# Performance work log

Hardware: AMD Instinct MI355X
Metric: run time of the kernel (lower is better)

The kernel has to match this reference:

```python
import jax, jax.numpy as jnp
import numpy as np

B, S, HID = 1, 2048, 2048
H, KVH, D, VD = 32, 8, 128, 128
R = 64  # rope_dim = head_dim * partial_rotary_factor, rounded down to even
N_REP = H // KVH
SCALE = D ** -0.5
NEG = -1e9


def _rotate_half(x):
    half = x.shape[-1] // 2
    return jnp.concatenate([-x[..., half:], x[..., :half]], axis=-1)


def setup_inputs() -> dict:
    key = jax.random.key(0)
    ks = jax.random.split(key, 8)
    hidden_states = jax.random.normal(ks[0], (B, S, HID), dtype=jnp.float32)
    # RoPE angles: standard inverse-frequency positional embedding of width R
    inv_freq = 1.0 / (10000.0 ** (np.arange(0, R, 2, dtype=np.float32) / R))
    pos = np.arange(S, dtype=np.float32)
    freqs = np.outer(pos, inv_freq)                       # [S, R/2]
    emb = np.concatenate([freqs, freqs], axis=-1)         # [S, R]
    cos = jnp.asarray(np.cos(emb))[None].repeat(B, axis=0)  # [B, S, R]
    sin = jnp.asarray(np.sin(emb))[None].repeat(B, axis=0)
    # additive causal mask [B, 1, S, S]
    causal = jnp.triu(jnp.full((S, S), NEG, dtype=jnp.float32), k=1)
    attention_mask = jnp.broadcast_to(causal[None, None], (B, 1, S, S))
    std = 0.02
    Wq = jax.random.normal(ks[1], (H * D, HID), dtype=jnp.float32) * std
    Wk = jax.random.normal(ks[2], (KVH * D, HID), dtype=jnp.float32) * std
    Wv = jax.random.normal(ks[3], (KVH * VD, HID), dtype=jnp.float32) * std
    Wo = jax.random.normal(ks[4], (HID, H * VD), dtype=jnp.float32) * std
    sink_bias = jax.random.normal(ks[5], (H,), dtype=jnp.float32) * 0.5
    return {"hidden_states": hidden_states, "cos": cos, "sin": sin,
            "attention_mask": attention_mask, "Wq": Wq, "Wk": Wk, "Wv": Wv,
            "Wo": Wo, "sink_bias": sink_bias}


def reference(hidden_states, cos, sin, attention_mask, Wq, Wk, Wv, Wo, sink_bias):
    b, s, _ = hidden_states.shape
    # projections -> [B, heads, S, dim]
    q = (hidden_states @ Wq.T).reshape(b, s, H, D).transpose(0, 2, 1, 3)
    k = (hidden_states @ Wk.T).reshape(b, s, KVH, D).transpose(0, 2, 1, 3)
    v = (hidden_states @ Wv.T).reshape(b, s, KVH, VD).transpose(0, 2, 1, 3)
    # partial RoPE on first R dims
    c = cos[:, None, :, :]  # [B,1,S,R]
    si = sin[:, None, :, :]
    q_r, q_n = q[..., :R], q[..., R:]
    k_r, k_n = k[..., :R], k[..., R:]
    q = jnp.concatenate([q_r * c + _rotate_half(q_r) * si, q_n], axis=-1)
    k = jnp.concatenate([k_r * c + _rotate_half(k_r) * si, k_n], axis=-1)
    # GQA: repeat kv heads
    k_rep = jnp.repeat(k, N_REP, axis=1)
    v_rep = jnp.repeat(v, N_REP, axis=1)
    scores = jnp.einsum('bhqd,bhkd->bhqk', q, k_rep) * SCALE + attention_mask
    # extra attention-sink logit column per head
    sinks = jnp.broadcast_to(sink_bias.reshape(1, H, 1, 1), (b, H, s, 1))
    aw = jnp.concatenate([scores, sinks], axis=-1)            # [B,H,S,S+1]
    probs = jax.nn.softmax(aw, axis=-1)[..., :-1]             # drop sink column
    out = jnp.einsum('bhqk,bhkd->bhqd', probs, v_rep)
    out = out.transpose(0, 2, 1, 3).reshape(b, s, H * VD)
    return out @ Wo.T
```

## Files before the change

### kernel.cpp

```cpp
#include <hip/hip_runtime.h>

typedef unsigned short u16;
typedef unsigned int   u32;
typedef __bf16  bf16x8 __attribute__((ext_vector_type(8)));
typedef float   f32x4  __attribute__((ext_vector_type(4)));
typedef float   f32x16 __attribute__((ext_vector_type(16)));
typedef u16     u16x4  __attribute__((ext_vector_type(4)));
typedef u16     u16x8  __attribute__((ext_vector_type(8)));
typedef u32     u32x4  __attribute__((ext_vector_type(4)));

#define S_LEN 2048
#define NH 32
#define NKVH 8
#define HD 128
#define QKVST 6144
#define AOST  4096
#define ATT_SCALE 0.08838834764831845f
#define LOG2E 1.4426950408889634f
#define QSC2 (ATT_SCALE * LOG2E)
#define RESCALE_THR2 11.5f

__device__ __forceinline__ u16 f2bf(float f){
  u32 u = __builtin_bit_cast(u32, f);
  u += 0x7FFFu + ((u >> 16) & 1u);
  return (u16)(u >> 16);
}
__device__ __forceinline__ u32 cvtpk(float lo, float hi){
  u32 d;
  asm("v_cvt_pk_bf16_f32 %0, %1, %2" : "=v"(d) : "v"(lo), "v"(hi));
  return d;
}
__device__ __forceinline__ void gload_lds16(const u16* g, u16* l){
  __builtin_amdgcn_global_load_lds(
      (const __attribute__((address_space(1))) void*)g,
      (__attribute__((address_space(3))) void*)l, 16, 0, 0);
}

__global__ void cvt_all_kernel(const f32x4* __restrict__ hs, const f32x4* __restrict__ wq,
                               const f32x4* __restrict__ wk, const f32x4* __restrict__ wv,
                               const f32x4* __restrict__ wo, u16x4* __restrict__ out){
  int i = blockIdx.x * 256 + threadIdx.x;
  const f32x4* src; int off;
  if      (i < 1048576){ src = hs; off = i; }
  else if (i < 3145728){ src = wq; off = i - 1048576; }
  else if (i < 3670016){ src = wk; off = i - 3145728; }
  else if (i < 4194304){ src = wv; off = i - 3670016; }
  else                 { src = wo; off = i - 4194304; }
  f32x4 v = src[off];
  u16x4 o;
  o[0] = f2bf(v[0]); o[1] = f2bf(v[1]); o[2] = f2bf(v[2]); o[3] = f2bf(v[3]);
  out[i] = o;
}

template<int OUT_BF16, int ROPE, int BM, int BN, int BK>
__global__ __launch_bounds__(256, 2)
void gemm_bt_kernel(const u16* __restrict__ X, const u16* __restrict__ W,
                    void* __restrict__ Cv, int M, int N, int K,
                    const float* __restrict__ cosv, const float* __restrict__ sinv){
  const int NS = BK / 32;
  __shared__ __align__(16) u16 As[2][NS][BM * 32];
  __shared__ __align__(16) u16 Bs[2][NS][BN * 32];
  const int MI = BM / 32, NJ = BN / 32;
  const int m0 = blockIdx.y * BM, n0 = blockIdx.x * BN;
  const int tid = threadIdx.x;
  const int wave = tid >> 6, lane = tid & 63;
  const int wm = wave >> 1, wn = wave & 1;
  const int g = lane >> 4, ln = lane & 15;
  const int r0 = tid >> 2;
  const int cc = (tid & 3) * 8;
  f32x4 acc[MI][NJ] = {};
  const u16* xa0 = X + (size_t)(m0 + r0) * K + cc;
  const u16* xa1 = X + (size_t)(m0 + r0 + 64) * K + cc;
  const u16* wb0 = W + (size_t)(n0 + r0) * K + cc;
  const u16* wb1 = W + (size_t)(n0 + r0 + 64) * K + cc;

  auto stage = [&](int buf, int k0){
    #pragma unroll
    for (int s = 0; s < NS; s++){
      const int kc = k0 + s * 32;
      gload_lds16(xa0 + kc, &As[buf][s][tid * 8]);
      if (BM == 128) gload_lds16(xa1 + kc, &As[buf][s][2048 + tid * 8]);
      gload_lds16(wb0 + kc, &Bs[buf][s][tid * 8]);
      if (BN == 128) gload_lds16(wb1 + kc, &Bs[buf][s][2048 + tid * 8]);
    }
  };

  stage(0, 0);
  __syncthreads();
  int cur = 0;
  for (int k0 = 0; k0 < K; k0 += BK){
    if (k0 + BK < K) stage(cur ^ 1, k0 + BK);
    #pragma unroll
    for (int s = 0; s < NS; s++){
      bf16x8 a[MI], b[NJ];
      #pragma unroll
      for (int f = 0; f < MI; f++) a[f] = *(const bf16x8*)&As[cur][s][(wm * (BM / 2) + f * 16 + ln) * 32 + g * 8];
      #pragma unroll
      for (int f = 0; f < NJ; f++) b[f] = *(const bf16x8*)&Bs[cur][s][(wn * (BN / 2) + f * 16 + ln) * 32 + g * 8];
      __builtin_amdgcn_s_setprio(1);
      #pragma unroll
      for (int i = 0; i < MI; i++)
        #pragma unroll
        for (int j = 0; j < NJ; j++)
          acc[i][j] = __builtin_amdgcn_mfma_f32_16x16x32_bf16(a[i], b[j], acc[i][j], 0, 0, 0);
      __builtin_amdgcn_s_setprio(0);
    }
    __syncthreads();
    cur ^= 1;
  }
  if (ROPE && BN == 128){
    if (wn == 0 && n0 < 5120){
      #pragma unroll
      for (int i = 0; i < MI; i++)
        #pragma unroll
        for (int r = 0; r < 4; r++){
          const int row = m0 + wm * (BM / 2) + i * 16 + g * 4 + r;
          #pragma unroll
          for (int j = 0; j < 2; j++){
            const int d = j * 16 + ln;
            float c  = cosv[row * 64 + d];
            float sn = sinv[row * 64 + d];
            float x0 = acc[i][j][r], x1 = acc[i][j + 2][r];
            acc[i][j][r]     = x0 * c - x1 * sn;
            acc[i][j + 2][r] = x1 * c + x0 * sn;
          }
        }
    }
    if (n0 < 4096){
      #pragma unroll
      for (int i = 0; i < MI; i++)
        #pragma unroll
        for (int j = 0; j < NJ; j++)
          #pragma unroll
          for (int r = 0; r < 4; r++) acc[i][j][r] *= QSC2;
    }
  }
  #pragma unroll
  for (int i = 0; i < MI; i++)
    #pragma unroll
    for (int j = 0; j < NJ; j++)
      #pragma unroll
      for (int r = 0; r < 4; r++){
        int row = m0 + wm * (BM / 2) + i * 16 + g * 4 + r;
        int col = n0 + wn * (BN / 2) + j * 16 + ln;
        if (OUT_BF16) ((u16*)Cv)[(size_t)row * N + col] = f2bf(acc[i][j][r]);
        else          ((float*)Cv)[(size_t)row * N + col] = acc[i][j][r];
      }
}

__global__ void vtrans_kernel(const u16* __restrict__ QKV, u16* __restrict__ VT){
  int idx = blockIdx.x * 256 + threadIdx.x;
  if (idx >= NKVH * HD * S_LEN) return;
  int s   = idx & (S_LEN - 1);
  int vd  = (idx >> 11) & (HD - 1);
  int kvh = idx >> 18;
  VT[idx] = QKV[(size_t)s * QKVST + 5120 + kvh * HD + vd];
}

__global__ __launch_bounds__(256, 2)
void attn_kernel(const u16* __restrict__ QKV, const u16* __restrict__ VT,
                 const float* __restrict__ sinkb, u16* __restrict__ AO){
  __shared__ __align__(16) u16 Ks[2][32 * 256];
  __shared__ __align__(16) u16 Vs[2][32 * 256];
  const int b    = blockIdx.x;
  const int kvh  = b & 7;
  const int head = kvh * 4 + ((b >> 3) & 3);
  const int slot = b >> 5;
  const int qt   = (slot < 8) ? (15 - slot) : (slot - 8);
  const int tid  = threadIdx.x;
  const int w    = tid >> 6;
  const int lane = tid & 63;
  const int l31  = lane & 31, hi = lane >> 5;
  const int q0   = qt * 128;
  const int qw   = q0 + w * 32;

  const u16* Kbase = QKV + 4096 + kvh * HD;
  const u16* Vbase = VT + (size_t)kvh * HD * S_LEN;

  auto stage = [&](int buf, int kt){
    const int k0 = kt * 64;
    #pragma unroll
    for (int p = 0; p < 4; p++){
      int idx = p * 256 + tid;
      int r = idx >> 5, c = idx & 31;
      int cs = c ^ r;
      int key = r * 2 + (cs >> 4), d8 = (cs & 15) * 8;
      gload_lds16(Kbase + (size_t)(k0 + key) * QKVST + d8, &Ks[buf][idx * 8]);
    }
    #pragma unroll
    for (int p = 0; p < 4; p++){
      int idx = p * 256 + tid;
      int r = idx >> 5, c = idx & 31;
      int cs = c ^ r;
      int vd = r * 4 + (cs >> 3), k8 = (cs & 7) * 8;
      gload_lds16(Vbase + (size_t)vd * S_LEN + k0 + k8, &Vs[buf][idx * 8]);
    }
  };

  bf16x8 qB[8];
  const u16* qrow = QKV + (size_t)(qw + l31) * QKVST + head * HD;
  #pragma unroll
  for (int t = 0; t < 8; t++) qB[t] = *(const bf16x8*)(qrow + t * 16 + hi * 8);

  float m  = sinkb[head] * LOG2E;
  float Ll = (hi == 0) ? 1.f : 0.f;
  f32x16 O[4] = {};

  const int nkt = 2 * qt + 2;
  stage(0, 0);
  __syncthreads();
  int cur = 0;

  for (int kt = 0; kt < nkt; kt++){
    const int k0 = kt * 64;
    if (kt + 1 < nkt) stage(cur ^ 1, kt + 1);

    if (k0 < qw + 32){
      const u16* Kc = Ks[cur];
      const u16* Vc = Vs[cur];
      f32x16 sc0 = {}, sc1 = {};
      const int krow0 = (l31 >> 1);
      const int kc0   = ((l31 & 1) << 4) | hi;
      __builtin_amdgcn_s_setprio(1);
      #pragma unroll
      for (int t = 0; t < 8; t++){
        bf16x8 ka0 = *(const bf16x8*)&Kc[krow0 * 256 + ((kc0 + 2 * t) ^ krow0) * 8];
        bf16x8 ka1 = *(const bf16x8*)&Kc[(16 + krow0) * 256 + ((kc0 + 2 * t) ^ (16 + krow0)) * 8];
        sc0 = __builtin_amdgcn_mfma_f32_32x32x16_bf16(ka0, qB[t], sc0, 0, 0, 0);
        sc1 = __builtin_amdgcn_mfma_f32_32x32x16_bf16(ka1, qB[t], sc1, 0, 0, 0);
      }
      __builtin_amdgcn_s_setprio(0);

      if (k0 + 63 > qw){
        const int qg = qw + l31;
        #pragma unroll
        for (int r = 0; r < 16; r++){
          int keyr = k0 + (r & 3) + 8 * (r >> 2) + 4 * hi;
          if (keyr      > qg) sc0[r] = -1e30f;
          if (keyr + 32 > qg) sc1[r] = -1e30f;
        }
      }
      float mx = sc0[0];
      #pragma unroll
      for (int r = 1; r < 16; r++) mx = fmaxf(mx, sc0[r]);
      #pragma unroll
      for (int r = 0; r < 16; r++) mx = fmaxf(mx, sc1[r]);
      mx = fmaxf(mx, __shfl_xor(mx, 32));
      if (!__all(mx <= m + RESCALE_THR2)){
        float mn = fmaxf(m, mx);
        float sf = exp2f(m - mn);
        m = mn;
        #pragma unroll
        for (int n = 0; n < 4; n++)
          #pragma unroll
          for (int r = 0; r < 16; r++) O[n][r] *= sf;
        Ll *= sf;
      }
      float p0[16], p1[16];
      #pragma unroll
      for (int r = 0; r < 16; r++){ p0[r] = exp2f(sc0[r] - m); Ll += p0[r]; }
      #pragma unroll
      for (int r = 0; r < 16; r++){ p1[r] = exp2f(sc1[r] - m); Ll += p1[r]; }

      __builtin_amdgcn_s_setprio(1);
      #pragma unroll
      for (int c = 0; c < 4; c++){
        const float* ps = (c & 2) ? p1 : p0;
        const int bb = (c & 1) * 8;
        u32 wa = cvtpk(ps[bb + 0], ps[bb + 1]);
        u32 wb = cvtpk(ps[bb + 2], ps[bb + 3]);
        u32 wc = cvtpk(ps[bb + 4], ps[bb + 5]);
        u32 wd = cvtpk(ps[bb + 6], ps[bb + 7]);
        asm("v_permlane32_swap_b32 %0, %1" : "+v"(wa), "+v"(wc));
        asm("v_permlane32_swap_b32 %0, %1" : "+v"(wb), "+v"(wd));
        u32x4 wv_; wv_[0] = wa; wv_[1] = wb; wv_[2] = wc; wv_[3] = wd;
        bf16x8 pf = __builtin_bit_cast(bf16x8, wv_);
        #pragma unroll
        for (int n = 0; n < 4; n++){
          const int vrow = n * 8 + (l31 >> 2);
          const int vcc  = ((l31 & 3) << 3) | (c << 1) | hi;
          bf16x8 va = *(const bf16x8*)&Vc[vrow * 256 + (vcc ^ vrow) * 8];
          O[n] = __builtin_amdgcn_mfma_f32_32x32x16_bf16(va, pf, O[n], 0, 0, 0);
        }
      }
      __builtin_amdgcn_s_setprio(0);
    }
    __syncthreads();
    cur ^= 1;
  }

  float l = Ll + __shfl_xor(Ll, 32);
  float inv = 1.f / l;
  u16* arena = &Ks[0][0];
  #pragma unroll
  for (int n = 0; n < 4; n++)
    #pragma unroll
    for (int r = 0; r < 16; r++){
      int vd = n * 32 + (r & 3) + 8 * (r >> 2) + 4 * hi;
      int ch = (vd >> 3) ^ (l31 & 15);
      arena[w * 4096 + l31 * 128 + ch * 8 + (vd & 7)] = f2bf(O[n][r] * inv);
    }
  __syncthreads();
  #pragma unroll
  for (int p = 0; p < 8; p++){
    int idx = p * 256 + tid;
    int row = idx >> 4, c = idx & 15;
    u16x8 v = *(const u16x8*)&arena[row * 128 + ((c ^ (row & 15)) * 8)];
    *(u16x8*)&AO[(size_t)(q0 + row) * AOST + head * HD + c * 8] = v;
  }
}

extern "C" void kernel_launch(void* const* d_in, const int* in_sizes, int n_in,
                              void* d_out, int out_size, void* d_ws, size_t ws_size,
                              hipStream_t stream){
  (void)in_sizes; (void)n_in; (void)out_size; (void)ws_size;
  const float* hs    = (const float*)d_in[0];
  const float* cosv  = (const float*)d_in[1];
  const float* sinv  = (const float*)d_in[2];
  const float* Wq    = (const float*)d_in[4];
  const float* Wk    = (const float*)d_in[5];
  const float* Wv    = (const float*)d_in[6];
  const float* Wo    = (const float*)d_in[7];
  const float* sinkb = (const float*)d_in[8];
  float* out = (float*)d_out;

  char* ws = (char*)d_ws;
  u16* XB    = (u16*)(ws);
  u16* WQKVB = (u16*)(ws + 8388608);
  u16* WOB   = (u16*)(ws + 33554432);
  u16* QKV   = (u16*)(ws + 50331648);
  u16* VT    = (u16*)(ws + 75497472);
  u16* AO    = (u16*)(ws + 79691776);

  cvt_all_kernel<<<24576, 256, 0, stream>>>((const f32x4*)hs, (const f32x4*)Wq,
                                            (const f32x4*)Wk, (const f32x4*)Wv,
                                            (const f32x4*)Wo, (u16x4*)ws);

  gemm_bt_kernel<1, 1, 128, 128, 32><<<dim3(48, 16), 256, 0, stream>>>(XB, WQKVB, QKV, 2048, 6144, 2048, cosv, sinv);

  vtrans_kernel<<<8192, 256, 0, stream>>>(QKV, VT);

  attn_kernel<<<dim3(512), 256, 0, stream>>>(QKV, VT, sinkb, AO);

  gemm_bt_kernel<0, 0, 128, 64, 64><<<dim3(32, 16), 256, 0, stream>>>(AO, WOB, out, 2048, 2048, 4096, nullptr, nullptr);
}
```

Before: 229.3 us.

## Split long causal query tiles across blocks with LSE merge for load balance

Each attention block now does a fixed amount of work. The long query tiles (qt 8..15) are split along the key dimension: one block handles keys 0..17 tiles and a second block handles the rest, then the second block also processes a short tile. The partial outputs are written in bf16 together with per-row log-sum-exp values into workspace reused from the XB area. A new merge kernel combines the two partials. This is meant to remove the tail imbalance of the causal workload, at the cost of an extra kernel launch, partial-output traffic and additional bf16 rounding.

```diff
diff --git a/kernel.cpp b/kernel.cpp
--- a/kernel.cpp
+++ b/kernel.cpp
@@ -19,11 +19,16 @@
 #define LOG2E 1.4426950408889634f
 #define QSC2 (ATT_SCALE * LOG2E)
 #define RESCALE_THR2 11.5f
+#define PARTSZ 16640
 
 __device__ __forceinline__ u16 f2bf(float f){
   u32 u = __builtin_bit_cast(u32, f);
   u += 0x7FFFu + ((u >> 16) & 1u);
   return (u16)(u >> 16);
+}
+__device__ __forceinline__ float bf2f(u16 h){
+  u32 u = ((u32)h) << 16;
+  return __builtin_bit_cast(float, u);
 }
 __device__ __forceinline__ u32 cvtpk(float lo, float hi){
   u32 d;
@@ -159,20 +164,20 @@
 
 __global__ __launch_bounds__(256, 2)
 void attn_kernel(const u16* __restrict__ QKV, const u16* __restrict__ VT,
-                 const float* __restrict__ sinkb, u16* __restrict__ AO){
+                 const float* __restrict__ sinkb, u16* __restrict__ AO,
+                 u16* __restrict__ PART){
   __shared__ __align__(16) u16 Ks[2][32 * 256];
   __shared__ __align__(16) u16 Vs[2][32 * 256];
   const int b    = blockIdx.x;
   const int kvh  = b & 7;
   const int head = kvh * 4 + ((b >> 3) & 3);
-  const int slot = b >> 5;
-  const int qt   = (slot < 8) ? (15 - slot) : (slot - 8);
+  const int p    = (b >> 5) & 7;
+  const int role = b >> 8;
+  const int qtL  = 15 - p;
   const int tid  = threadIdx.x;
   const int w    = tid >> 6;
   const int lane = tid & 63;
   const int l31  = lane & 31, hi = lane >> 5;
-  const int q0   = qt * 128;
-  const int qw   = q0 + w * 32;
 
   const u16* Kbase = QKV + 4096 + kvh * HD;
   const u16* Vbase = VT + (size_t)kvh * HD * S_LEN;
@@ -180,16 +185,16 @@
   auto stage = [&](int buf, int kt){
     const int k0 = kt * 64;
     #pragma unroll
-    for (int p = 0; p < 4; p++){
-      int idx = p * 256 + tid;
+    for (int pp = 0; pp < 4; pp++){
+      int idx = pp * 256 + tid;
       int r = idx >> 5, c = idx & 31;
       int cs = c ^ r;
       int key = r * 2 + (cs >> 4), d8 = (cs & 15) * 8;
       gload_lds16(Kbase + (size_t)(k0 + key) * QKVST + d8, &Ks[buf][idx * 8]);
     }
     #pragma unroll
-    for (int p = 0; p < 4; p++){
-      int idx = p * 256 + tid;
+    for (int pp = 0; pp < 4; pp++){
+      int idx = pp * 256 + tid;
       int r = idx >> 5, c = idx & 31;
       int cs = c ^ r;
       int vd = r * 4 + (cs >> 3), k8 = (cs & 7) * 8;
@@ -197,116 +202,183 @@
     }
   };
 
+  const float sb2 = sinkb[head] * LOG2E;
   bf16x8 qB[8];
-  const u16* qrow = QKV + (size_t)(qw + l31) * QKVST + head * HD;
+  float m, Ll;
+  f32x16 O[4];
+
+  auto load_q = [&](int q0){
+    const int qw = q0 + w * 32;
+    const u16* qrow = QKV + (size_t)(qw + l31) * QKVST + head * HD;
+    #pragma unroll
+    for (int t = 0; t < 8; t++) qB[t] = *(const bf16x8*)(qrow + t * 16 + hi * 8);
+    #pragma unroll
+    for (int n = 0; n < 4; n++) O[n] = f32x16{};
+  };
+
+  auto do_tile = [&](int cur, int k0, int qw){
+    const u16* Kc = Ks[cur];
+    const u16* Vc = Vs[cur];
+    f32x16 sc0 = {}, sc1 = {};
+    const int krow0 = (l31 >> 1);
+    const int kc0   = ((l31 & 1) << 4) | hi;
+    __builtin_amdgcn_s_setprio(1);
+    #pragma unroll
+    for (int t = 0; t < 8; t++){
+      bf16x8 ka0 = *(const bf16x8*)&Kc[krow0 * 256 + ((kc0 + 2 * t) ^ krow0) * 8];
+      bf16x8 ka1 = *(const bf16x8*)&Kc[(16 + krow0) * 256 + ((kc0 + 2 * t) ^ (16 + krow0)) * 8];
+      sc0 = __builtin_amdgcn_mfma_f32_32x32x16_bf16(ka0, qB[t], sc0, 0, 0, 0);
+      sc1 = __builtin_amdgcn_mfma_f32_32x32x16_bf16(ka1, qB[t], sc1, 0, 0, 0);
+    }
+    __builtin_amdgcn_s_setprio(0);
+
+    if (k0 + 63 > qw){
+      const int qg = qw + l31;
+      #pragma unroll
+      for (int r = 0; r < 16; r++){
+        int keyr = k0 + (r & 3) + 8 * (r >> 2) + 4 * hi;
+        if (keyr      > qg) sc0[r] = -1e30f;
+        if (keyr + 32 > qg) sc1[r] = -1e30f;
+      }
+    }
+    float mx = sc0[0];
+    #pragma unroll
+    for (int r = 1; r < 16; r++) mx = fmaxf(mx, sc0[r]);
+    #pragma unroll
+    for (int r = 0; r < 16; r++) mx = fmaxf(mx, sc1[r]);
+    mx = fmaxf(mx, __shfl_xor(mx, 32));
+    if (!__all(mx <= m + RESCALE_THR2)){
+      float mn = fmaxf(m, mx);
+      float sf = exp2f(m - mn);
+      m = mn;
+      #pragma unroll
+      for (int n = 0; n < 4; n++)
+        #pragma unroll
+        for (int r = 0; r < 16; r++) O[n][r] *= sf;
+      Ll *= sf;
+    }
+    float p0[16], p1[16];
+    #pragma unroll
+    for (int r = 0; r < 16; r++){ p0[r] = exp2f(sc0[r] - m); Ll += p0[r]; }
+    #pragma unroll
+    for (int r = 0; r < 16; r++){ p1[r] = exp2f(sc1[r] - m); Ll += p1[r]; }
+
+    __builtin_amdgcn_s_setprio(1);
+    #pragma unroll
+    for (int c = 0; c < 4; c++){
+      const float* ps = (c & 2) ? p1 : p0;
+      const int bb = (c & 1) * 8;
+      u32 wa = cvtpk(ps[bb + 0], ps[bb + 1]);
+      u32 wb = cvtpk(ps[bb + 2], ps[bb + 3]);
+      u32 wc = cvtpk(ps[bb + 4], ps[bb + 5]);
+      u32 wd = cvtpk(ps[bb + 6], ps[bb + 7]);
+      asm("v_permlane32_swap_b32 %0, %1" : "+v"(wa), "+v"(wc));
+      asm("v_permlane32_swap_b32 %0, %1" : "+v"(wb), "+v"(wd));
+      u32x4 wv_; wv_[0] = wa; wv_[1] = wb; wv_[2] = wc; wv_[3] = wd;
+      bf16x8 pf = __builtin_bit_cast(bf16x8, wv_);
+      #pragma unroll
+      for (int n = 0; n < 4; n++){
+        const int vrow = n * 8 + (l31 >> 2);
+        const int vcc  = ((l31 & 3) << 3) | (c << 1) | hi;
+        bf16x8 va = *(const bf16x8*)&Vc[vrow * 256 + (vcc ^ vrow) * 8];
+        O[n] = __builtin_amdgcn_mfma_f32_32x32x16_bf16(va, pf, O[n], 0, 0, 0);
+      }
+    }
+    __builtin_amdgcn_s_setprio(0);
+  };
+
+  auto run = [&](int q0, int kt0, int kt1){
+    const int qw = q0 + w * 32;
+    stage(0, kt0);
+    __syncthreads();
+    int cur = 0;
+    for (int kt = kt0; kt < kt1; kt++){
+      if (kt + 1 < kt1) stage(cur ^ 1, kt + 1);
+      if (kt * 64 < qw + 32) do_tile(cur, kt * 64, qw);
+      __syncthreads();
+      cur ^= 1;
+    }
+  };
+
+  auto epilogue = [&](int q0, bool final_, int rr_){
+    float l = Ll + __shfl_xor(Ll, 32);
+    float inv, lse;
+    if (l > 0.f){ inv = 1.f / l; lse = m + __log2f(l); }
+    else        { inv = 0.f;     lse = -1e30f; }
+    u16* arena = &Ks[0][0];
+    #pragma unroll
+    for (int n = 0; n < 4; n++)
+      #pragma unroll
+      for (int r = 0; r < 16; r++){
+        int vd = n * 32 + (r & 3) + 8 * (r >> 2) + 4 * hi;
+        int ch = (vd >> 3) ^ (l31 & 15);
+        arena[w * 4096 + l31 * 128 + ch * 8 + (vd & 7)] = f2bf(O[n][r] * inv);
+      }
+    __syncthreads();
+    if (final_){
+      #pragma unroll
+      for (int pp = 0; pp < 8; pp++){
+        int idx = pp * 256 + tid;
+        int row = idx >> 4, c = idx & 15;
+        u16x8 v = *(const u16x8*)&arena[row * 128 + ((c ^ (row & 15)) * 8)];
+        *(u16x8*)&AO[(size_t)(q0 + row) * AOST + head * HD + c * 8] = v;
+      }
+    } else {
+      u16* base = PART + (size_t)((head * 8 + p) * 2 + rr_) * PARTSZ;
+      #pragma unroll
+      for (int pp = 0; pp < 8; pp++){
+        int idx = pp * 256 + tid;
+        int row = idx >> 4, c = idx & 15;
+        u16x8 v = *(const u16x8*)&arena[row * 128 + ((c ^ (row & 15)) * 8)];
+        *(u16x8*)&base[row * 128 + c * 8] = v;
+      }
+      if (hi == 0) ((float*)(base + 16384))[w * 32 + l31] = lse;
+    }
+    __syncthreads();
+  };
+
+  const int q0L = qtL * 128;
+  if (role == 0){
+    load_q(q0L);
+    m = sb2; Ll = (hi == 0) ? 1.f : 0.f;
+    run(q0L, 0, 17);
+    epilogue(q0L, false, 0);
+  } else {
+    load_q(q0L);
+    m = -3.0e38f; Ll = 0.f;
+    run(q0L, 17, 32 - 2 * p);
+    epilogue(q0L, false, 1);
+    const int q0S = p * 128;
+    load_q(q0S);
+    m = sb2; Ll = (hi == 0) ? 1.f : 0.f;
+    run(q0S, 0, 2 * p + 2);
+    epilogue(q0S, true, 0);
+  }
+}
+
+__global__ void merge_kernel(const u16* __restrict__ PART, u16* __restrict__ AO){
+  const int sidx = blockIdx.x;
+  const int h = sidx >> 3, p = sidx & 7;
+  const int q0 = (15 - p) * 128;
+  const u16* A = PART + (size_t)(sidx * 2 + 0) * PARTSZ;
+  const u16* B = PART + (size_t)(sidx * 2 + 1) * PARTSZ;
+  const float* lseA = (const float*)(A + 16384);
+  const float* lseB = (const float*)(B + 16384);
   #pragma unroll
-  for (int t = 0; t < 8; t++) qB[t] = *(const bf16x8*)(qrow + t * 16 + hi * 8);
-
-  float m  = sinkb[head] * LOG2E;
-  float Ll = (hi == 0) ? 1.f : 0.f;
-  f32x16 O[4] = {};
-
-  const int nkt = 2 * qt + 2;
-  stage(0, 0);
-  __syncthreads();
-  int cur = 0;
-
-  for (int kt = 0; kt < nkt; kt++){
-    const int k0 = kt * 64;
-    if (kt + 1 < nkt) stage(cur ^ 1, kt + 1);
-
-    if (k0 < qw + 32){
-      const u16* Kc = Ks[cur];
-      const u16* Vc = Vs[cur];
-      f32x16 sc0 = {}, sc1 = {};
-      const int krow0 = (l31 >> 1);
-      const int kc0   = ((l31 & 1) << 4) | hi;
-      __builtin_amdgcn_s_setprio(1);
-      #pragma unroll
-      for (int t = 0; t < 8; t++){
-        bf16x8 ka0 = *(const bf16x8*)&Kc[krow0 * 256 + ((kc0 + 2 * t) ^ krow0) * 8];
-        bf16x8 ka1 = *(const bf16x8*)&Kc[(16 + krow0) * 256 + ((kc0 + 2 * t) ^ (16 + krow0)) * 8];
-        sc0 = __builtin_amdgcn_mfma_f32_32x32x16_bf16(ka0, qB[t], sc0, 0, 0, 0);
-        sc1 = __builtin_amdgcn_mfma_f32_32x32x16_bf16(ka1, qB[t], sc1, 0, 0, 0);
-      }
-      __builtin_amdgcn_s_setprio(0);
-
-      if (k0 + 63 > qw){
-        const int qg = qw + l31;
-        #pragma unroll
-        for (int r = 0; r < 16; r++){
-          int keyr = k0 + (r & 3) + 8 * (r >> 2) + 4 * hi;
-          if (keyr      > qg) sc0[r] = -1e30f;
-          if (keyr + 32 > qg) sc1[r] = -1e30f;
-        }
-      }
-      float mx = sc0[0];
-      #pragma unroll
-      for (int r = 1; r < 16; r++) mx = fmaxf(mx, sc0[r]);
-      #pragma unroll
-      for (int r = 0; r < 16; r++) mx = fmaxf(mx, sc1[r]);
-      mx = fmaxf(mx, __shfl_xor(mx, 32));
-      if (!__all(mx <= m + RESCALE_THR2)){
-        float mn = fmaxf(m, mx);
-        float sf = exp2f(m - mn);
-        m = mn;
-        #pragma unroll
-        for (int n = 0; n < 4; n++)
-          #pragma unroll
-          for (int r = 0; r < 16; r++) O[n][r] *= sf;
-        Ll *= sf;
-      }
-      float p0[16], p1[16];
-      #pragma unroll
-      for (int r = 0; r < 16; r++){ p0[r] = exp2f(sc0[r] - m); Ll += p0[r]; }
-      #pragma unroll
-      for (int r = 0; r < 16; r++){ p1[r] = exp2f(sc1[r] - m); Ll += p1[r]; }
-
-      __builtin_amdgcn_s_setprio(1);
-      #pragma unroll
-      for (int c = 0; c < 4; c++){
-        const float* ps = (c & 2) ? p1 : p0;
-        const int bb = (c & 1) * 8;
-        u32 wa = cvtpk(ps[bb + 0], ps[bb + 1]);
-        u32 wb = cvtpk(ps[bb + 2], ps[bb + 3]);
-        u32 wc = cvtpk(ps[bb + 4], ps[bb + 5]);
-        u32 wd = cvtpk(ps[bb + 6], ps[bb + 7]);
-        asm("v_permlane32_swap_b32 %0, %1" : "+v"(wa), "+v"(wc));
-        asm("v_permlane32_swap_b32 %0, %1" : "+v"(wb), "+v"(wd));
-        u32x4 wv_; wv_[0] = wa; wv_[1] = wb; wv_[2] = wc; wv_[3] = wd;
-        bf16x8 pf = __builtin_bit_cast(bf16x8, wv_);
-        #pragma unroll
-        for (int n = 0; n < 4; n++){
-          const int vrow = n * 8 + (l31 >> 2);
-          const int vcc  = ((l31 & 3) << 3) | (c << 1) | hi;
-          bf16x8 va = *(const bf16x8*)&Vc[vrow * 256 + (vcc ^ vrow) * 8];
-          O[n] = __builtin_amdgcn_mfma_f32_32x32x16_bf16(va, pf, O[n], 0, 0, 0);
-        }
-      }
-      __builtin_amdgcn_s_setprio(0);
-    }
-    __syncthreads();
-    cur ^= 1;
-  }
-
-  float l = Ll + __shfl_xor(Ll, 32);
-  float inv = 1.f / l;
-  u16* arena = &Ks[0][0];
-  #pragma unroll
-  for (int n = 0; n < 4; n++)
-    #pragma unroll
-    for (int r = 0; r < 16; r++){
-      int vd = n * 32 + (r & 3) + 8 * (r >> 2) + 4 * hi;
-      int ch = (vd >> 3) ^ (l31 & 15);
-      arena[w * 4096 + l31 * 128 + ch * 8 + (vd & 7)] = f2bf(O[n][r] * inv);
-    }
-  __syncthreads();
-  #pragma unroll
-  for (int p = 0; p < 8; p++){
-    int idx = p * 256 + tid;
-    int row = idx >> 4, c = idx & 15;
-    u16x8 v = *(const u16x8*)&arena[row * 128 + ((c ^ (row & 15)) * 8)];
-    *(u16x8*)&AO[(size_t)(q0 + row) * AOST + head * HD + c * 8] = v;
+  for (int it = 0; it < 8; it++){
+    int idx = it * 256 + threadIdx.x;
+    int row = idx >> 4, c = (idx & 15) * 8;
+    float la = lseA[row], lb = lseB[row];
+    float mx = fmaxf(la, lb);
+    float wa = exp2f(la - mx), wb = exp2f(lb - mx);
+    float inv = 1.f / (wa + wb);
+    u16x8 va = *(const u16x8*)&A[row * 128 + c];
+    u16x8 vb = *(const u16x8*)&B[row * 128 + c];
+    u16x8 o;
+    #pragma unroll
+    for (int j = 0; j < 8; j++)
+      o[j] = f2bf((bf2f(va[j]) * wa + bf2f(vb[j]) * wb) * inv);
+    *(u16x8*)&AO[(size_t)(q0 + row) * AOST + h * HD + c] = o;
   }
 }
 
@@ -331,6 +403,7 @@
   u16* QKV   = (u16*)(ws + 50331648);
   u16* VT    = (u16*)(ws + 75497472);
   u16* AO    = (u16*)(ws + 79691776);
+  u16* PART  = (u16*)(ws);
 
   cvt_all_kernel<<<24576, 256, 0, stream>>>((const f32x4*)hs, (const f32x4*)Wq,
                                             (const f32x4*)Wk, (const f32x4*)Wv,
@@ -340,7 +413,9 @@
 
   vtrans_kernel<<<8192, 256, 0, stream>>>(QKV, VT);
 
-  attn_kernel<<<dim3(512), 256, 0, stream>>>(QKV, VT, sinkb, AO);
+  attn_kernel<<<dim3(512), 256, 0, stream>>>(QKV, VT, sinkb, AO, PART);
+
+  merge_kernel<<<dim3(256), 256, 0, stream>>>(PART, AO);
 
   gemm_bt_kernel<0, 0, 128, 64, 64><<<dim3(32, 16), 256, 0, stream>>>(AO, WOB, out, 2048, 2048, 4096, nullptr, nullptr);
 }
```

Result: faster. 224.8 us (-2.0%).
